# Performance work log

Measured on AMD Instinct MI355X. Metric: run time of the kernel, lower is better.

The kernel has to match this reference:

```python
import jax, jax.numpy as jnp
import numpy as np

IN_F = 1024
OUT_F = 1024
B, S = 8, 4096


def _pack_ternary(tern):
    # encoding: -1 -> 0, 0 -> 1, +1 -> 2; 4 values per byte, matching torch pack_ternary_weights
    enc = (tern + 1.0).astype(jnp.int32).reshape(-1)  # length divisible by 4 here
    return (enc[0::4] | (enc[1::4] << 2) | (enc[2::4] << 4) | (enc[3::4] << 6)).astype(jnp.int32)


def setup_inputs() -> dict:
    key = jax.random.key(0)
    kx, kw = jax.random.split(key)
    x = jax.random.normal(kx, (B, S, IN_F), dtype=jnp.float32)
    w = jax.random.normal(kw, (OUT_F, IN_F), dtype=jnp.float32) * 0.02
    # quantize_weights_158bit
    scale = jnp.maximum(jnp.mean(jnp.abs(w)), 1e-5)
    wn = w / scale
    tern = jnp.sign(wn) * (jnp.abs(wn) > 0.5).astype(jnp.float32)
    packed = _pack_ternary(tern)
    bias = jnp.zeros((OUT_F,), dtype=jnp.float32)
    return {"x": x, "packed_weight": packed, "weight_scale": scale.reshape(1), "bias": bias}


def reference(x, packed_weight, weight_scale, bias):
    n = OUT_F * IN_F
    shifts = jnp.array([0, 2, 4, 6], dtype=jnp.int32)
    # Faithful to original unpack_ternary_weights: concatenate bit-planes, then truncate.
    # (This is a permutation of the packed order, replicated deliberately.)
    enc = ((packed_weight[None, :] >> shifts[:, None]) & 3).reshape(-1)[:n]
    w = (enc.astype(jnp.float32) - 1.0).reshape(OUT_F, IN_F) * weight_scale  # dequant ternary
    # training path: INT8 per-token activation fake-quant
    act_scale = 127.0 / jnp.maximum(jnp.max(jnp.abs(x), axis=-1, keepdims=True), 1e-5)
    x_dq = jnp.clip(jnp.round(x * act_scale), -128.0, 127.0) / act_scale
    return jnp.einsum('bsi,oi->bso', x_dq, w) + bias
```

## Files before the change

kernel.cpp:

```cpp
#include <hip/hip_runtime.h>
#include <hip/hip_bf16.h>
#include <stdint.h>

typedef int i32x4 __attribute__((ext_vector_type(4)));

constexpr int IN_F = 1024;
constexpr int OUT_F = 1024;
constexpr int M_TOT = 8 * 4096;
constexpr int K_TOT = IN_F;
constexpr int N_TOT = OUT_F;

__global__ __launch_bounds__(256) void quant_kernel(
    const float* __restrict__ x,
    const float* __restrict__ wscale,
    int8_t* __restrict__ q,
    float* __restrict__ inv_row)
{
    const int row = blockIdx.x;
    const int t = threadIdx.x;
    const float4 v = reinterpret_cast<const float4*>(x + (size_t)row * IN_F)[t];
    float m = fmaxf(fmaxf(fabsf(v.x), fabsf(v.y)), fmaxf(fabsf(v.z), fabsf(v.w)));
    #pragma unroll
    for (int off = 32; off > 0; off >>= 1)
        m = fmaxf(m, __shfl_xor(m, off));
    __shared__ float smax[4];
    if ((t & 63) == 0) smax[t >> 6] = m;
    __syncthreads();
    m = fmaxf(fmaxf(smax[0], smax[1]), fmaxf(smax[2], smax[3]));
    const float a = fmaxf(m, 1e-5f);
    const float as = 127.0f / a;

    char4 o;
    o.x = (char)(int)fminf(fmaxf(rintf(v.x * as), -128.0f), 127.0f);
    o.y = (char)(int)fminf(fmaxf(rintf(v.y * as), -128.0f), 127.0f);
    o.z = (char)(int)fminf(fmaxf(rintf(v.z * as), -128.0f), 127.0f);
    o.w = (char)(int)fminf(fmaxf(rintf(v.w * as), -128.0f), 127.0f);
    reinterpret_cast<char4*>(q + (size_t)row * IN_F)[t] = o;
    if (t == 0) inv_row[row] = (a / 127.0f) * wscale[0];
}

__global__ __launch_bounds__(256) void unpack_kernel(
    const int* __restrict__ packed,
    int8_t* __restrict__ wt2)
{
    const int o = blockIdx.x;
    const int t = threadIdx.x;
    const int k0 = t * 4;
    const int sh = (o >> 8) * 2;
    const int pbase = ((o & 255) << 10) + k0;
    const int4 pw = *reinterpret_cast<const int4*>(packed + pbase);
    char4 r;
    r.x = (char)(((pw.x >> sh) & 3) - 1);
    r.y = (char)(((pw.y >> sh) & 3) - 1);
    r.z = (char)(((pw.z >> sh) & 3) - 1);
    r.w = (char)(((pw.w >> sh) & 3) - 1);
    const int addr = (k0 >> 6) * 65536 + o * 64 + ((k0 >> 4) & 3) * 16 + (k0 & 15);
    *reinterpret_cast<char4*>(wt2 + addr) = r;
}

constexpr int BM = 128, BN = 256, BK = 128;
constexpr int NT = K_TOT / BK;

__global__ __launch_bounds__(512, 4) void gemm_kernel(
    const int8_t* __restrict__ qa,
    const int8_t* __restrict__ wb2,
    const float* __restrict__ inv_row,
    const float* __restrict__ bias,
    float* __restrict__ out)
{
    int bid = blockIdx.x;
    bid = (bid & 7) * ((int)gridDim.x >> 3) + (bid >> 3);
    const int tm = bid >> 2;
    const int tn = bid & 3;

    const int tid = threadIdx.x;
    const int lane = tid & 63;
    const int wid = tid >> 6;
    const int wr = wid >> 2;
    const int wc = wid & 3;

    __shared__ int8_t ldsA[3][128 * 128];

    const int rowA0 = tm * BM;
    const int rowB0 = tn * BN;
    const int frow = lane & 15;
    const int fq = lane >> 4;

    i32x4 acc[4][4] = {};

    const int rl0 = tid >> 3;
    const int scc0 = (tid & 7) ^ (rl0 & 7);
    const int8_t* srcA0 = qa + (size_t)(rowA0 + rl0) * K_TOT + scc0 * 16;
    const int dA0 = tid * 16, dA1 = (512 + tid) * 16;

    auto stageA = [&](int slot, int kt) {
        __builtin_amdgcn_global_load_lds(
            (const __attribute__((address_space(1))) void*)(srcA0 + kt * BK),
            (__attribute__((address_space(3))) void*)&ldsA[slot][dA0], 16, 0, 0);
        __builtin_amdgcn_global_load_lds(
            (const __attribute__((address_space(1))) void*)(srcA0 + (size_t)64 * K_TOT + kt * BK),
            (__attribute__((address_space(3))) void*)&ldsA[slot][dA1], 16, 0, 0);
    };

    auto ldA = [&](int slot, int mf, int ks) -> i32x4 {
        const int local = wr * 64 + mf * 16 + frow;
        const int ch = (ks * 4 + fq) ^ (local & 7);
        return *reinterpret_cast<const i32x4*>(&ldsA[slot][local * 128 + ch * 16]);
    };

    const int8_t* wbBase = wb2 + (size_t)(rowB0 + wc * 64 + frow) * 64 + fq * 16;
    i32x4 bF[4][2];
    auto loadB = [&](int T) {
        #pragma unroll
        for (int nf = 0; nf < 4; ++nf)
            #pragma unroll
            for (int ks = 0; ks < 2; ++ks)
                bF[nf][ks] = *reinterpret_cast<const i32x4*>(
                    wbBase + (size_t)(T * 2 + ks) * 65536 + nf * 1024);
    };

    stageA(0, 0);
    stageA(1, 1);
    loadB(0);

    #pragma unroll 1
    for (int T = 0; T < NT; ++T) {
        const int sa = T % 3;
        if (T < NT - 1) asm volatile("s_waitcnt vmcnt(10)" ::: "memory");
        else            asm volatile("s_waitcnt vmcnt(0)" ::: "memory");
        __builtin_amdgcn_s_barrier();

        i32x4 aF[4];

        #pragma unroll
        for (int mf = 0; mf < 4; ++mf) aF[mf] = ldA(sa, mf, 0);
        if (T + 2 < NT) stageA((T + 2) % 3, T + 2);
        asm volatile("s_waitcnt lgkmcnt(0)" ::: "memory");
        __builtin_amdgcn_sched_barrier(0);
        __builtin_amdgcn_s_setprio(1);
        #pragma unroll
        for (int mf = 0; mf < 4; ++mf)
            #pragma unroll
            for (int nf = 0; nf < 4; ++nf)
                acc[mf][nf] = __builtin_amdgcn_mfma_i32_16x16x64_i8(
                    aF[mf], bF[nf][0], acc[mf][nf], 0, 0, 0);
        __builtin_amdgcn_s_setprio(0);

        #pragma unroll
        for (int mf = 0; mf < 4; ++mf) aF[mf] = ldA(sa, mf, 1);
        asm volatile("s_waitcnt lgkmcnt(0)" ::: "memory");
        __builtin_amdgcn_sched_barrier(0);
        __builtin_amdgcn_s_setprio(1);
        #pragma unroll
        for (int mf = 0; mf < 4; ++mf)
            #pragma unroll
            for (int nf = 0; nf < 4; ++nf)
                acc[mf][nf] = __builtin_amdgcn_mfma_i32_16x16x64_i8(
                    aF[mf], bF[nf][1], acc[mf][nf], 0, 0, 0);
        __builtin_amdgcn_s_setprio(0);

        if (T + 1 < NT) loadB(T + 1);
    }

    #pragma unroll
    for (int mf = 0; mf < 4; ++mf) {
        #pragma unroll
        for (int j = 0; j < 4; ++j) {
            const int gm = rowA0 + wr * 64 + mf * 16 + fq * 4 + j;
            const float sc = inv_row[gm];
            #pragma unroll
            for (int nf = 0; nf < 4; ++nf) {
                const int gn = rowB0 + wc * 64 + nf * 16 + frow;
                out[(size_t)gm * N_TOT + gn] = (float)acc[mf][nf][j] * sc + bias[gn];
            }
        }
    }
}

extern "C" void kernel_launch(void* const* d_in, const int* in_sizes, int n_in,
                              void* d_out, int out_size, void* d_ws, size_t ws_size,
                              hipStream_t stream) {
    const float* x = (const float*)d_in[0];
    const int* packed = (const int*)d_in[1];
    const float* wscale = (const float*)d_in[2];
    const float* bias = (const float*)d_in[3];
    float* out = (float*)d_out;

    int8_t* q = (int8_t*)d_ws;
    int8_t* wt2 = (int8_t*)((char*)d_ws + (size_t)M_TOT * K_TOT);
    float* inv_row = (float*)((char*)d_ws + (size_t)M_TOT * K_TOT + (size_t)N_TOT * K_TOT);

    quant_kernel<<<M_TOT, 256, 0, stream>>>(x, wscale, q, inv_row);
    unpack_kernel<<<OUT_F, 256, 0, stream>>>(packed, wt2);
    gemm_kernel<<<(M_TOT / BM) * (N_TOT / BN), 512, 0, stream>>>(q, wt2, inv_row, bias, out);
}
```

Baseline: 94.15 us.

## Fuse activation quantization into GEMM with whole-row-block int8 tiles in LDS

Drops the separate quant kernel and the int8 activation buffer in global memory. Each block now reads 128 rows of x, computes the per-row max and quantizes them straight into a 128KB swizzled LDS tile. It then computes all 1024 output columns in two halves, streaming weight fragments from global into registers, and writes results with nontemporal stores. This removes the global write and re-read of the quantized activations and one launch. In exchange, occupancy drops to roughly one block per CU, and the quantization and MFMA phases no longer overlap within a CU.

Result: slower. 99.00 us (+5.1%).

```diff
diff --git a/kernel.cpp b/kernel.cpp
--- a/kernel.cpp
+++ b/kernel.cpp
@@ -7,45 +7,15 @@
 constexpr int IN_F = 1024;
 constexpr int OUT_F = 1024;
 constexpr int M_TOT = 8 * 4096;
-constexpr int K_TOT = IN_F;
-constexpr int N_TOT = OUT_F;
-
-__global__ __launch_bounds__(256) void quant_kernel(
-    const float* __restrict__ x,
-    const float* __restrict__ wscale,
-    int8_t* __restrict__ q,
-    float* __restrict__ inv_row)
-{
-    const int row = blockIdx.x;
-    const int t = threadIdx.x;
-    const float4 v = reinterpret_cast<const float4*>(x + (size_t)row * IN_F)[t];
-    float m = fmaxf(fmaxf(fabsf(v.x), fabsf(v.y)), fmaxf(fabsf(v.z), fabsf(v.w)));
-    #pragma unroll
-    for (int off = 32; off > 0; off >>= 1)
-        m = fmaxf(m, __shfl_xor(m, off));
-    __shared__ float smax[4];
-    if ((t & 63) == 0) smax[t >> 6] = m;
-    __syncthreads();
-    m = fmaxf(fmaxf(smax[0], smax[1]), fmaxf(smax[2], smax[3]));
-    const float a = fmaxf(m, 1e-5f);
-    const float as = 127.0f / a;
-
-    char4 o;
-    o.x = (char)(int)fminf(fmaxf(rintf(v.x * as), -128.0f), 127.0f);
-    o.y = (char)(int)fminf(fmaxf(rintf(v.y * as), -128.0f), 127.0f);
-    o.z = (char)(int)fminf(fmaxf(rintf(v.z * as), -128.0f), 127.0f);
-    o.w = (char)(int)fminf(fmaxf(rintf(v.w * as), -128.0f), 127.0f);
-    reinterpret_cast<char4*>(q + (size_t)row * IN_F)[t] = o;
-    if (t == 0) inv_row[row] = (a / 127.0f) * wscale[0];
-}
+constexpr int K_TOT = 1024;
+constexpr int N_TOT = 1024;
 
 __global__ __launch_bounds__(256) void unpack_kernel(
     const int* __restrict__ packed,
     int8_t* __restrict__ wt2)
 {
     const int o = blockIdx.x;
-    const int t = threadIdx.x;
-    const int k0 = t * 4;
+    const int k0 = threadIdx.x * 4;
     const int sh = (o >> 8) * 2;
     const int pbase = ((o & 255) << 10) + k0;
     const int4 pw = *reinterpret_cast<const int4*>(packed + pbase);
@@ -58,120 +28,138 @@
     *reinterpret_cast<char4*>(wt2 + addr) = r;
 }
 
-constexpr int BM = 128, BN = 256, BK = 128;
-constexpr int NT = K_TOT / BK;
-
-__global__ __launch_bounds__(512, 4) void gemm_kernel(
-    const int8_t* __restrict__ qa,
-    const int8_t* __restrict__ wb2,
-    const float* __restrict__ inv_row,
+__global__ __launch_bounds__(512, 2) void fused_kernel(
+    const float* __restrict__ x,
+    const int8_t* __restrict__ wt2,
+    const float* __restrict__ wscale,
     const float* __restrict__ bias,
     float* __restrict__ out)
 {
-    int bid = blockIdx.x;
-    bid = (bid & 7) * ((int)gridDim.x >> 3) + (bid >> 3);
-    const int tm = bid >> 2;
-    const int tn = bid & 3;
-
     const int tid = threadIdx.x;
     const int lane = tid & 63;
     const int wid = tid >> 6;
     const int wr = wid >> 2;
     const int wc = wid & 3;
-
-    __shared__ int8_t ldsA[3][128 * 128];
-
-    const int rowA0 = tm * BM;
-    const int rowB0 = tn * BN;
     const int frow = lane & 15;
     const int fq = lane >> 4;
+    const int row0 = blockIdx.x * 128;
 
-    i32x4 acc[4][4] = {};
+    __shared__ int8_t qT[128 * 1024];
+    __shared__ float scl[128];
 
-    const int rl0 = tid >> 3;
-    const int scc0 = (tid & 7) ^ (rl0 & 7);
-    const int8_t* srcA0 = qa + (size_t)(rowA0 + rl0) * K_TOT + scc0 * 16;
-    const int dA0 = tid * 16, dA1 = (512 + tid) * 16;
+    const float wsc = wscale[0];
+    const int c8 = lane & 7;
+    #pragma unroll
+    for (int g = 0; g < 2; ++g) {
+        const int lr = wid * 16 + g * 8 + (lane >> 3);
+        const float4* xr = reinterpret_cast<const float4*>(x + (size_t)(row0 + lr) * IN_F);
+        float m = 0.f;
+        #pragma unroll 4
+        for (int j = 0; j < 32; ++j) {
+            const float4 v = xr[c8 + 8 * j];
+            m = fmaxf(m, fmaxf(fmaxf(fabsf(v.x), fabsf(v.y)),
+                               fmaxf(fabsf(v.z), fabsf(v.w))));
+        }
+        m = fmaxf(m, __shfl_xor(m, 1));
+        m = fmaxf(m, __shfl_xor(m, 2));
+        m = fmaxf(m, __shfl_xor(m, 4));
+        const float a = fmaxf(m, 1e-5f);
+        const float as = 127.0f / a;
+        if (c8 == 0) scl[lr] = (a / 127.0f) * wsc;
+        #pragma unroll 2
+        for (int jj = 0; jj < 8; ++jj) {
+            const int ci = c8 + 8 * jj;
+            i32x4 o4;
+            #pragma unroll
+            for (int u = 0; u < 4; ++u) {
+                const float4 v = xr[ci * 4 + u];
+                const int b0 = (int)fminf(fmaxf(rintf(v.x * as), -128.f), 127.f) & 255;
+                const int b1 = (int)fminf(fmaxf(rintf(v.y * as), -128.f), 127.f) & 255;
+                const int b2 = (int)fminf(fmaxf(rintf(v.z * as), -128.f), 127.f) & 255;
+                const int b3 = (int)fminf(fmaxf(rintf(v.w * as), -128.f), 127.f) & 255;
+                o4[u] = b0 | (b1 << 8) | (b2 << 16) | (b3 << 24);
+            }
+            const int sc16 = ci ^ (lr & 7);
+            *reinterpret_cast<i32x4*>(&qT[lr * 1024 + sc16 * 16]) = o4;
+        }
+    }
+    __syncthreads();
 
-    auto stageA = [&](int slot, int kt) {
-        __builtin_amdgcn_global_load_lds(
-            (const __attribute__((address_space(1))) void*)(srcA0 + kt * BK),
-            (__attribute__((address_space(3))) void*)&ldsA[slot][dA0], 16, 0, 0);
-        __builtin_amdgcn_global_load_lds(
-            (const __attribute__((address_space(1))) void*)(srcA0 + (size_t)64 * K_TOT + kt * BK),
-            (__attribute__((address_space(3))) void*)&ldsA[slot][dA1], 16, 0, 0);
+    auto ldA = [&](int kt, int mf) -> i32x4 {
+        const int lrow = wr * 64 + mf * 16 + frow;
+        const int c = kt * 4 + fq;
+        return *reinterpret_cast<const i32x4*>(&qT[lrow * 1024 + (c ^ (lrow & 7)) * 16]);
     };
-
-    auto ldA = [&](int slot, int mf, int ks) -> i32x4 {
-        const int local = wr * 64 + mf * 16 + frow;
-        const int ch = (ks * 4 + fq) ^ (local & 7);
-        return *reinterpret_cast<const i32x4*>(&ldsA[slot][local * 128 + ch * 16]);
-    };
-
-    const int8_t* wbBase = wb2 + (size_t)(rowB0 + wc * 64 + frow) * 64 + fq * 16;
-    i32x4 bF[4][2];
-    auto loadB = [&](int T) {
-        #pragma unroll
-        for (int nf = 0; nf < 4; ++nf)
-            #pragma unroll
-            for (int ks = 0; ks < 2; ++ks)
-                bF[nf][ks] = *reinterpret_cast<const i32x4*>(
-                    wbBase + (size_t)(T * 2 + ks) * 65536 + nf * 1024);
-    };
-
-    stageA(0, 0);
-    stageA(1, 1);
-    loadB(0);
+    const int8_t* wbB = wt2 + (size_t)(wc * 128 + frow) * 64 + fq * 16;
 
     #pragma unroll 1
-    for (int T = 0; T < NT; ++T) {
-        const int sa = T % 3;
-        if (T < NT - 1) asm volatile("s_waitcnt vmcnt(10)" ::: "memory");
-        else            asm volatile("s_waitcnt vmcnt(0)" ::: "memory");
-        __builtin_amdgcn_s_barrier();
+    for (int half = 0; half < 2; ++half) {
+        const int8_t* wbH = wbB + (size_t)half * 512 * 64;
+        i32x4 acc[4][8] = {};
+        i32x4 bX[8], bY[8];
+        #pragma unroll
+        for (int nf = 0; nf < 8; ++nf)
+            bX[nf] = *reinterpret_cast<const i32x4*>(wbH + 0 * 65536 + nf * 1024);
+        #pragma unroll
+        for (int nf = 0; nf < 8; ++nf)
+            bY[nf] = *reinterpret_cast<const i32x4*>(wbH + 1 * 65536 + nf * 1024);
 
-        i32x4 aF[4];
+        #pragma unroll 1
+        for (int kt = 0; kt < 16; kt += 2) {
+            {
+                i32x4 aF[4];
+                #pragma unroll
+                for (int mf = 0; mf < 4; ++mf) aF[mf] = ldA(kt, mf);
+                __builtin_amdgcn_s_setprio(1);
+                #pragma unroll
+                for (int mf = 0; mf < 4; ++mf)
+                    #pragma unroll
+                    for (int nf = 0; nf < 8; ++nf)
+                        acc[mf][nf] = __builtin_amdgcn_mfma_i32_16x16x64_i8(
+                            aF[mf], bX[nf], acc[mf][nf], 0, 0, 0);
+                __builtin_amdgcn_s_setprio(0);
+                if (kt + 2 < 16) {
+                    #pragma unroll
+                    for (int nf = 0; nf < 8; ++nf)
+                        bX[nf] = *reinterpret_cast<const i32x4*>(
+                            wbH + (size_t)(kt + 2) * 65536 + nf * 1024);
+                }
+            }
+            {
+                i32x4 aF[4];
+                #pragma unroll
+                for (int mf = 0; mf < 4; ++mf) aF[mf] = ldA(kt + 1, mf);
+                __builtin_amdgcn_s_setprio(1);
+                #pragma unroll
+                for (int mf = 0; mf < 4; ++mf)
+                    #pragma unroll
+                    for (int nf = 0; nf < 8; ++nf)
+                        acc[mf][nf] = __builtin_amdgcn_mfma_i32_16x16x64_i8(
+                            aF[mf], bY[nf], acc[mf][nf], 0, 0, 0);
+                __builtin_amdgcn_s_setprio(0);
+                if (kt + 3 < 16) {
+                    #pragma unroll
+                    for (int nf = 0; nf < 8; ++nf)
+                        bY[nf] = *reinterpret_cast<const i32x4*>(
+                            wbH + (size_t)(kt + 3) * 65536 + nf * 1024);
+                }
+            }
+        }
 
         #pragma unroll
-        for (int mf = 0; mf < 4; ++mf) aF[mf] = ldA(sa, mf, 0);
-        if (T + 2 < NT) stageA((T + 2) % 3, T + 2);
-        asm volatile("s_waitcnt lgkmcnt(0)" ::: "memory");
-        __builtin_amdgcn_sched_barrier(0);
-        __builtin_amdgcn_s_setprio(1);
-        #pragma unroll
-        for (int mf = 0; mf < 4; ++mf)
+        for (int mf = 0; mf < 4; ++mf) {
             #pragma unroll
-            for (int nf = 0; nf < 4; ++nf)
-                acc[mf][nf] = __builtin_amdgcn_mfma_i32_16x16x64_i8(
-                    aF[mf], bF[nf][0], acc[mf][nf], 0, 0, 0);
-        __builtin_amdgcn_s_setprio(0);
-
-        #pragma unroll
-        for (int mf = 0; mf < 4; ++mf) aF[mf] = ldA(sa, mf, 1);
-        asm volatile("s_waitcnt lgkmcnt(0)" ::: "memory");
-        __builtin_amdgcn_sched_barrier(0);
-        __builtin_amdgcn_s_setprio(1);
-        #pragma unroll
-        for (int mf = 0; mf < 4; ++mf)
-            #pragma unroll
-            for (int nf = 0; nf < 4; ++nf)
-                acc[mf][nf] = __builtin_amdgcn_mfma_i32_16x16x64_i8(
-                    aF[mf], bF[nf][1], acc[mf][nf], 0, 0, 0);
-        __builtin_amdgcn_s_setprio(0);
-
-        if (T + 1 < NT) loadB(T + 1);
-    }
-
-    #pragma unroll
-    for (int mf = 0; mf < 4; ++mf) {
-        #pragma unroll
-        for (int j = 0; j < 4; ++j) {
-            const int gm = rowA0 + wr * 64 + mf * 16 + fq * 4 + j;
-            const float sc = inv_row[gm];
-            #pragma unroll
-            for (int nf = 0; nf < 4; ++nf) {
-                const int gn = rowB0 + wc * 64 + nf * 16 + frow;
-                out[(size_t)gm * N_TOT + gn] = (float)acc[mf][nf][j] * sc + bias[gn];
+            for (int j = 0; j < 4; ++j) {
+                const int lrow = wr * 64 + mf * 16 + fq * 4 + j;
+                const int gm = row0 + lrow;
+                const float sc = scl[lrow];
+                #pragma unroll
+                for (int nf = 0; nf < 8; ++nf) {
+                    const int gn = half * 512 + wc * 128 + nf * 16 + frow;
+                    __builtin_nontemporal_store(
+                        (float)acc[mf][nf][j] * sc + bias[gn],
+                        &out[(size_t)gm * N_TOT + gn]);
+                }
             }
         }
     }
@@ -186,11 +174,8 @@
     const float* bias = (const float*)d_in[3];
     float* out = (float*)d_out;
 
-    int8_t* q = (int8_t*)d_ws;
-    int8_t* wt2 = (int8_t*)((char*)d_ws + (size_t)M_TOT * K_TOT);
-    float* inv_row = (float*)((char*)d_ws + (size_t)M_TOT * K_TOT + (size_t)N_TOT * K_TOT);
+    int8_t* wt2 = (int8_t*)d_ws;
 
-    quant_kernel<<<M_TOT, 256, 0, stream>>>(x, wscale, q, inv_row);
     unpack_kernel<<<OUT_F, 256, 0, stream>>>(packed, wt2);
-    gemm_kernel<<<(M_TOT / BM) * (N_TOT / BN), 512, 0, stream>>>(q, wt2, inv_row, bias, out);
+    fused_kernel<<<M_TOT / 128, 512, 0, stream>>>(x, wt2, wscale, bias, out);
 }
```
